# Performance work log

Measured on AMD Instinct MI355X. Metric: run time of the kernel, lower is better.

The kernel has to match this reference:

```python
import jax, jax.numpy as jnp
import numpy as np

def setup_inputs() -> dict:
    key = jax.random.key(0)
    x = jax.random.normal(key, (4, 1, 192, 224, 192), dtype=jnp.float32)
    return {"x": x}

def reference(x) -> jnp.ndarray:
    # Zero-pad each spatial dim by 1 (matches F.conv3d padding=1),
    # then take central differences: out[i] = (x[i+1] - x[i-1]) / 2.
    xp = jnp.pad(x, ((0, 0), (0, 0), (1, 1), (1, 1), (1, 1)))
    half = jnp.asarray(0.5, dtype=x.dtype)
    dz = (xp[:, :, 2:, 1:-1, 1:-1] - xp[:, :, :-2, 1:-1, 1:-1]) * half  # D axis (dZ kernel)
    dy = (xp[:, :, 1:-1, 2:, 1:-1] - xp[:, :, 1:-1, :-2, 1:-1]) * half  # H axis (dY kernel)
    dx = (xp[:, :, 1:-1, 1:-1, 2:] - xp[:, :, 1:-1, 1:-1, :-2]) * half  # W axis (dX kernel)
    return jnp.abs(dx) + jnp.abs(dy) + jnp.abs(dz)
```

## Files before the change

### kernel.cpp

```cpp
#include <hip/hip_runtime.h>


constexpr int W = 192, H = 224, D = 192, B = 4;
constexpr int W4     = W / 4;
constexpr int PLANE4 = W4 * H;
constexpr int BY     = 4;
constexpr int CH     = 2;
constexpr int ZC     = D / CH;
constexpr int YT     = H / BY;
constexpr int GRID   = B * ZC * YT;
constexpr int PERX   = GRID / 8;

typedef float f32x4 __attribute__((ext_vector_type(4)));

__global__ __launch_bounds__(192) void grad3d_kernel(
    const float* __restrict__ in, float* __restrict__ out) {
    int bid = blockIdx.x;
    int sid = (bid & 7) * PERX + (bid >> 3);
    const int yt = sid % YT; sid /= YT;
    const int zc = sid % ZC; sid /= ZC;
    const int b  = sid;

    const int xv = threadIdx.x;
    const int r  = yt * BY + threadIdx.y;
    const int z0 = zc * CH;

    const f32x4* __restrict__ in4 = (const f32x4*)in;
    f32x4* __restrict__ out4 = (f32x4*)out;
    const f32x4 zf = {0.f, 0.f, 0.f, 0.f};

    const bool has_l  = (xv > 0);
    const bool has_r  = (xv < W4 - 1);
    const bool has_ym = (r > 0);
    const bool has_yp = (r < H - 1);

    const int i0 = (b * D + z0) * PLANE4 + r * W4 + xv;
    const int i1 = i0 + PLANE4;

    f32x4 czm = (z0 > 0)     ? in4[i0 - PLANE4] : zf;
    f32x4 c0  =                in4[i0];
    f32x4 c1  =                in4[i1];
    f32x4 czp = (z0 + 2 < D) ? in4[i1 + PLANE4] : zf;
    f32x4 ym0 = has_ym ? in4[i0 - W4] : zf;
    f32x4 yp0 = has_yp ? in4[i0 + W4] : zf;
    f32x4 ym1 = has_ym ? in4[i1 - W4] : zf;
    f32x4 yp1 = has_yp ? in4[i1 + W4] : zf;
    float l0  = has_l ? in[i0 * 4 - 1] : 0.f;
    float r0e = has_r ? in[i0 * 4 + 4] : 0.f;
    float l1  = has_l ? in[i1 * 4 - 1] : 0.f;
    float r1e = has_r ? in[i1 * 4 + 4] : 0.f;

    f32x4 o0, o1;
    o0.x = fabsf((c0.y - l0  ) * .5f) + fabsf((yp0.x - ym0.x) * .5f) + fabsf((c1.x - czm.x) * .5f);
    o0.y = fabsf((c0.z - c0.x) * .5f) + fabsf((yp0.y - ym0.y) * .5f) + fabsf((c1.y - czm.y) * .5f);
    o0.z = fabsf((c0.w - c0.y) * .5f) + fabsf((yp0.z - ym0.z) * .5f) + fabsf((c1.z - czm.z) * .5f);
    o0.w = fabsf((r0e  - c0.z) * .5f) + fabsf((yp0.w - ym0.w) * .5f) + fabsf((c1.w - czm.w) * .5f);
    o1.x = fabsf((c1.y - l1  ) * .5f) + fabsf((yp1.x - ym1.x) * .5f) + fabsf((czp.x - c0.x) * .5f);
    o1.y = fabsf((c1.z - c1.x) * .5f) + fabsf((yp1.y - ym1.y) * .5f) + fabsf((czp.y - c0.y) * .5f);
    o1.z = fabsf((c1.w - c1.y) * .5f) + fabsf((yp1.z - ym1.z) * .5f) + fabsf((czp.z - c0.z) * .5f);
    o1.w = fabsf((r1e  - c1.z) * .5f) + fabsf((yp1.w - ym1.w) * .5f) + fabsf((czp.w - c0.w) * .5f);

    __builtin_nontemporal_store(o0, out4 + i0);
    __builtin_nontemporal_store(o1, out4 + i1);
}

extern "C" void kernel_launch(void* const* d_in, const int* in_sizes, int n_in,
                              void* d_out, int out_size, void* d_ws, size_t ws_size,
                              hipStream_t stream) {
    const float* x = (const float*)d_in[0];
    float* out     = (float*)d_out;
    dim3 block(W4, BY);
    grad3d_kernel<<<GRID, block, 0, stream>>>(x, out);
}
```

Before: 242.1 us.

## Stage halo tile in LDS via direct global-to-LDS loads for 3D stencil

Each block now stages an 8x10 plane halo tile (6 z-slices plus halos, 8 rows plus halos, full width) into shared memory using global_load_lds async loads, then computes 6 z-planes per thread from LDS. This cuts the redundant global reads of neighbour rows and planes that the register-only version issued. In exchange it adds a block-wide barrier and about 60 KB of LDS per block, which limits occupancy, and the load and compute phases no longer overlap within a block.

```diff
diff --git a/kernel.cpp b/kernel.cpp
--- a/kernel.cpp
+++ b/kernel.cpp
@@ -2,66 +2,100 @@
 
 
 constexpr int W = 192, H = 224, D = 192, B = 4;
-constexpr int W4     = W / 4;
-constexpr int PLANE4 = W4 * H;
-constexpr int BY     = 4;
-constexpr int CH     = 2;
-constexpr int ZC     = D / CH;
-constexpr int YT     = H / BY;
-constexpr int GRID   = B * ZC * YT;
-constexpr int PERX   = GRID / 8;
+constexpr int W4   = W / 4;
+constexpr int ZT   = 6, YT = 8;
+constexpr int ZP   = ZT + 2;
+constexpr int YP   = YT + 2;
+constexpr int ROWB = W * 4;
+constexpr int PLB  = YP * ROWB;
+constexpr int LDSB = ZP * PLB;
+constexpr int NZ   = D / ZT;
+constexpr int NY   = H / YT;
+constexpr int GRID = B * NZ * NY;
+constexpr int PERX = GRID / 8;
 
 typedef float f32x4 __attribute__((ext_vector_type(4)));
+typedef __attribute__((address_space(3))) unsigned int       lds_u32;
+typedef __attribute__((address_space(1))) const unsigned int gbl_u32;
 
-__global__ __launch_bounds__(192) void grad3d_kernel(
+__global__ __launch_bounds__(384) void grad3d_kernel(
     const float* __restrict__ in, float* __restrict__ out) {
+    __shared__ float s[LDSB / 4];
+
     int bid = blockIdx.x;
     int sid = (bid & 7) * PERX + (bid >> 3);
-    const int yt = sid % YT; sid /= YT;
-    const int zc = sid % ZC; sid /= ZC;
+    const int yt = sid % NY; sid /= NY;
+    const int zc = sid % NZ; sid /= NZ;
     const int b  = sid;
 
-    const int xv = threadIdx.x;
-    const int r  = yt * BY + threadIdx.y;
-    const int z0 = zc * CH;
+    const int xv   = threadIdx.x;
+    const int y    = threadIdx.y;
+    const int flat = y * W4 + xv;
+    const int wv   = flat >> 6;
+    const int lane = flat & 63;
 
-    const f32x4* __restrict__ in4 = (const f32x4*)in;
-    f32x4* __restrict__ out4 = (f32x4*)out;
+    const int y0 = yt * YT;
+    const int z0 = zc * ZT;
+    const bool ybot = (y0 == 0);
+    const bool ytop = (y0 + YT == H);
+
+    f32x4* s4 = (f32x4*)s;
     const f32x4 zf = {0.f, 0.f, 0.f, 0.f};
 
-    const bool has_l  = (xv > 0);
-    const bool has_r  = (xv < W4 - 1);
-    const bool has_ym = (r > 0);
-    const bool has_yp = (r < H - 1);
+    if (z0 == 0)
+        for (int i = flat; i < PLB / 16; i += 384) s4[i] = zf;
+    if (z0 + ZT == D)
+        for (int i = flat; i < PLB / 16; i += 384) s4[(LDSB - PLB) / 16 + i] = zf;
+    if (ybot)
+        s4[y * (PLB / 16) + xv] = zf;
+    if (ytop)
+        s4[y * (PLB / 16) + (YP - 1) * W4 + xv] = zf;
 
-    const int i0 = (b * D + z0) * PLANE4 + r * W4 + xv;
-    const int i1 = i0 + PLANE4;
+    const char* inb = (const char*)in;
+    for (int c = wv; c < 64; c += 6) {
+        const int zz = c >> 3;
+        const int j  = c & 7;
+        const int gz = z0 - 1 + zz;
+        if (gz < 0 || gz >= D) continue;
+        const int p = (j << 10) + (lane << 4);
+        bool ok = (p < PLB);
+        if (ybot && p < ROWB)       ok = false;
+        if (ytop && p >= PLB - ROWB) ok = false;
+        if (ok) {
+            const char* g = inb + (size_t)((b * D + gz) * H + (y0 - 1)) * ROWB + p;
+            unsigned int* l = (unsigned int*)((char*)s + zz * PLB + (j << 10));
+            __builtin_amdgcn_global_load_lds((gbl_u32*)g, (lds_u32*)l, 16, 0, 0);
+        }
+    }
 
-    f32x4 czm = (z0 > 0)     ? in4[i0 - PLANE4] : zf;
-    f32x4 c0  =                in4[i0];
-    f32x4 c1  =                in4[i1];
-    f32x4 czp = (z0 + 2 < D) ? in4[i1 + PLANE4] : zf;
-    f32x4 ym0 = has_ym ? in4[i0 - W4] : zf;
-    f32x4 yp0 = has_yp ? in4[i0 + W4] : zf;
-    f32x4 ym1 = has_ym ? in4[i1 - W4] : zf;
-    f32x4 yp1 = has_yp ? in4[i1 + W4] : zf;
-    float l0  = has_l ? in[i0 * 4 - 1] : 0.f;
-    float r0e = has_r ? in[i0 * 4 + 4] : 0.f;
-    float l1  = has_l ? in[i1 * 4 - 1] : 0.f;
-    float r1e = has_r ? in[i1 * 4 + 4] : 0.f;
+    __syncthreads();
 
-    f32x4 o0, o1;
-    o0.x = fabsf((c0.y - l0  ) * .5f) + fabsf((yp0.x - ym0.x) * .5f) + fabsf((c1.x - czm.x) * .5f);
-    o0.y = fabsf((c0.z - c0.x) * .5f) + fabsf((yp0.y - ym0.y) * .5f) + fabsf((c1.y - czm.y) * .5f);
-    o0.z = fabsf((c0.w - c0.y) * .5f) + fabsf((yp0.z - ym0.z) * .5f) + fabsf((c1.z - czm.z) * .5f);
-    o0.w = fabsf((r0e  - c0.z) * .5f) + fabsf((yp0.w - ym0.w) * .5f) + fabsf((c1.w - czm.w) * .5f);
-    o1.x = fabsf((c1.y - l1  ) * .5f) + fabsf((yp1.x - ym1.x) * .5f) + fabsf((czp.x - c0.x) * .5f);
-    o1.y = fabsf((c1.z - c1.x) * .5f) + fabsf((yp1.y - ym1.y) * .5f) + fabsf((czp.y - c0.y) * .5f);
-    o1.z = fabsf((c1.w - c1.y) * .5f) + fabsf((yp1.z - ym1.z) * .5f) + fabsf((czp.z - c0.z) * .5f);
-    o1.w = fabsf((r1e  - c1.z) * .5f) + fabsf((yp1.w - ym1.w) * .5f) + fabsf((czp.w - c0.w) * .5f);
+    f32x4* out4 = (f32x4*)out;
+    constexpr int rowf = W;
+    constexpr int plf  = YP * W;
+    int ci = (YP + (y + 1)) * rowf + 4 * xv;
+    size_t oi = ((size_t)(b * D + z0) * H + (y0 + y)) * W4 + xv;
 
-    __builtin_nontemporal_store(o0, out4 + i0);
-    __builtin_nontemporal_store(o1, out4 + i1);
+#pragma unroll
+    for (int z = 0; z < ZT; ++z) {
+        f32x4 cc = *(const f32x4*)&s[ci];
+        f32x4 ym = *(const f32x4*)&s[ci - rowf];
+        f32x4 yp = *(const f32x4*)&s[ci + rowf];
+        f32x4 zm = *(const f32x4*)&s[ci - plf];
+        f32x4 zp = *(const f32x4*)&s[ci + plf];
+        float l  = (xv > 0)      ? s[ci - 1] : 0.f;
+        float r  = (xv < W4 - 1) ? s[ci + 4] : 0.f;
+
+        f32x4 o;
+        o.x = fabsf((cc.y - l   ) * .5f) + fabsf((yp.x - ym.x) * .5f) + fabsf((zp.x - zm.x) * .5f);
+        o.y = fabsf((cc.z - cc.x) * .5f) + fabsf((yp.y - ym.y) * .5f) + fabsf((zp.y - zm.y) * .5f);
+        o.z = fabsf((cc.w - cc.y) * .5f) + fabsf((yp.z - ym.z) * .5f) + fabsf((zp.z - zm.z) * .5f);
+        o.w = fabsf((r    - cc.z) * .5f) + fabsf((yp.w - ym.w) * .5f) + fabsf((zp.w - zm.w) * .5f);
+        __builtin_nontemporal_store(o, out4 + oi);
+
+        ci += plf;
+        oi += (size_t)H * W4;
+    }
 }
 
 extern "C" void kernel_launch(void* const* d_in, const int* in_sizes, int n_in,
@@ -69,6 +103,6 @@
                               hipStream_t stream) {
     const float* x = (const float*)d_in[0];
     float* out     = (float*)d_out;
-    dim3 block(W4, BY);
+    dim3 block(W4, YT);
     grad3d_kernel<<<GRID, block, 0, stream>>>(x, out);
 }
```

Result: faster. 231.8 us (-4.2%).

## Stream z-planes through an LDS ring buffer with async global_load_lds prefetch

Applied to the files above, without the earlier changes.

Replaces the one-shot per-thread stencil with blocks that march 16 z-planes over a 14-row y tile. Each plane is loaded once into a 4-slot LDS ring with direct global-to-LDS loads, prefetched two planes ahead, and reused for neighbor reads, with lane shuffles supplying the x neighbors. The goal is to cut redundant global reads (z and y halos) and overlap loads with compute. The cost is manual vmcnt waits, two barriers per plane, and fewer, longer-running blocks.

```diff
diff --git a/kernel.cpp b/kernel.cpp
--- a/kernel.cpp
+++ b/kernel.cpp
@@ -3,65 +3,125 @@
 
 constexpr int W = 192, H = 224, D = 192, B = 4;
 constexpr int W4     = W / 4;
-constexpr int PLANE4 = W4 * H;
-constexpr int BY     = 4;
-constexpr int CH     = 2;
-constexpr int ZC     = D / CH;
-constexpr int YT     = H / BY;
-constexpr int GRID   = B * ZC * YT;
+constexpr int YT     = 14;
+constexpr int YR     = YT + 2;
+constexpr int ROWB   = W * 4;
+constexpr int SLOTB  = YR * ROWB;
+constexpr int SLOTFL = SLOTB / 4;
+constexpr int SLOTF4 = SLOTB / 16;
+constexpr int ZL     = 16;
+constexpr int NYT    = H / YT;
+constexpr int NZC    = D / ZL;
+constexpr int GRID   = B * NYT * NZC;
 constexpr int PERX   = GRID / 8;
+constexpr int NTHR   = 256;
+constexpr int NF4    = YT * W4;
 
 typedef float f32x4 __attribute__((ext_vector_type(4)));
+typedef __attribute__((address_space(3))) unsigned int       lds_u32;
+typedef __attribute__((address_space(1))) const unsigned int gbl_u32;
 
-__global__ __launch_bounds__(192) void grad3d_kernel(
+#define WAITV(N) asm volatile("s_waitcnt vmcnt(" #N ")" ::: "memory")
+#define WAITLG   asm volatile("s_waitcnt lgkmcnt(0)" ::: "memory")
+#define BARR     asm volatile("s_barrier" ::: "memory")
+
+__global__ __launch_bounds__(NTHR) void grad3d_kernel(
     const float* __restrict__ in, float* __restrict__ out) {
+    __shared__ float s[4 * SLOTFL];
+
     int bid = blockIdx.x;
     int sid = (bid & 7) * PERX + (bid >> 3);
-    const int yt = sid % YT; sid /= YT;
-    const int zc = sid % ZC; sid /= ZC;
-    const int b  = sid;
+    const int ytile = sid % NYT; sid /= NYT;
+    const int zc    = sid % NZC; sid /= NZC;
+    const int b     = sid;
 
-    const int xv = threadIdx.x;
-    const int r  = yt * BY + threadIdx.y;
-    const int z0 = zc * CH;
+    const int tid  = threadIdx.x;
+    const int wv   = tid >> 6;
+    const int lane = tid & 63;
+    const int z0   = zc * ZL;
+    const int y0   = ytile * YT;
+    const bool ybot = (ytile == 0), ytop = (ytile == NYT - 1);
 
-    const f32x4* __restrict__ in4 = (const f32x4*)in;
-    f32x4* __restrict__ out4 = (f32x4*)out;
+    f32x4* s4 = (f32x4*)s;
+    f32x4* out4 = (f32x4*)out;
     const f32x4 zf = {0.f, 0.f, 0.f, 0.f};
+    const char* inb = (const char*)in;
 
-    const bool has_l  = (xv > 0);
-    const bool has_r  = (xv < W4 - 1);
-    const bool has_ym = (r > 0);
-    const bool has_yp = (r < H - 1);
+    if (ybot) for (int i = tid; i < 4 * W4; i += NTHR)
+        s4[(i / W4) * SLOTF4 + (i % W4)] = zf;
+    if (ytop) for (int i = tid; i < 4 * W4; i += NTHR)
+        s4[(i / W4) * SLOTF4 + (YR - 1) * W4 + (i % W4)] = zf;
 
-    const int i0 = (b * D + z0) * PLANE4 + r * W4 + xv;
-    const int i1 = i0 + PLANE4;
+    auto STAGE = [&](int q) {
+        const int sl = (q + 4) & 3;
+        if (q < 0 || q >= D) {
+            #pragma unroll
+            for (int k = 0; k < 3; ++k)
+                s4[sl * SLOTF4 + k * NTHR + tid] = zf;
+            return;
+        }
+        const char* gbase = inb + (size_t)((b * D + q) * H + (y0 - 1)) * ROWB;
+        char* lbase = (char*)s + sl * SLOTB;
+        #pragma unroll
+        for (int k = 0; k < 3; ++k) {
+            const int c   = 3 * wv + k;
+            const int off = (c << 10) + (lane << 4);
+            bool ok = true;
+            if (ybot && off < ROWB)         ok = false;
+            if (ytop && off >= SLOTB - ROWB) ok = false;
+            if (ok)
+                __builtin_amdgcn_global_load_lds(
+                    (gbl_u32*)(gbase + off),
+                    (lds_u32*)(lbase + (c << 10)), 16, 0, 0);
+        }
+    };
 
-    f32x4 czm = (z0 > 0)     ? in4[i0 - PLANE4] : zf;
-    f32x4 c0  =                in4[i0];
-    f32x4 c1  =                in4[i1];
-    f32x4 czp = (z0 + 2 < D) ? in4[i1 + PLANE4] : zf;
-    f32x4 ym0 = has_ym ? in4[i0 - W4] : zf;
-    f32x4 yp0 = has_yp ? in4[i0 + W4] : zf;
-    f32x4 ym1 = has_ym ? in4[i1 - W4] : zf;
-    f32x4 yp1 = has_yp ? in4[i1 + W4] : zf;
-    float l0  = has_l ? in[i0 * 4 - 1] : 0.f;
-    float r0e = has_r ? in[i0 * 4 + 4] : 0.f;
-    float l1  = has_l ? in[i1 * 4 - 1] : 0.f;
-    float r1e = has_r ? in[i1 * 4 + 4] : 0.f;
+    STAGE(z0 - 1);
+    STAGE(z0);
+    STAGE(z0 + 1);
 
-    f32x4 o0, o1;
-    o0.x = fabsf((c0.y - l0  ) * .5f) + fabsf((yp0.x - ym0.x) * .5f) + fabsf((c1.x - czm.x) * .5f);
-    o0.y = fabsf((c0.z - c0.x) * .5f) + fabsf((yp0.y - ym0.y) * .5f) + fabsf((c1.y - czm.y) * .5f);
-    o0.z = fabsf((c0.w - c0.y) * .5f) + fabsf((yp0.z - ym0.z) * .5f) + fabsf((c1.z - czm.z) * .5f);
-    o0.w = fabsf((r0e  - c0.z) * .5f) + fabsf((yp0.w - ym0.w) * .5f) + fabsf((c1.w - czm.w) * .5f);
-    o1.x = fabsf((c1.y - l1  ) * .5f) + fabsf((yp1.x - ym1.x) * .5f) + fabsf((czp.x - c0.x) * .5f);
-    o1.y = fabsf((c1.z - c1.x) * .5f) + fabsf((yp1.y - ym1.y) * .5f) + fabsf((czp.y - c0.y) * .5f);
-    o1.z = fabsf((c1.w - c1.y) * .5f) + fabsf((yp1.z - ym1.z) * .5f) + fabsf((czp.z - c0.z) * .5f);
-    o1.w = fabsf((r1e  - c1.z) * .5f) + fabsf((yp1.w - ym1.w) * .5f) + fabsf((czp.w - c0.w) * .5f);
+    for (int t = 0; t < ZL; ++t) {
+        const int z = z0 + t;
+        const int q = z + 2;
+        const bool inr = (q < D);
+        STAGE(q);
+        if (t == 0)      WAITV(3);
+        else if (inr)    WAITV(5);
+        else             WAITV(2);
+        WAITLG;
+        BARR;
 
-    __builtin_nontemporal_store(o0, out4 + i0);
-    __builtin_nontemporal_store(o1, out4 + i1);
+        const int szm = (z + 3) & 3, sz = z & 3, szp = (z + 1) & 3;
+        #pragma unroll
+        for (int it = 0; it < 3; ++it) {
+            const int f = it * NTHR + tid;
+            if (f < NF4) {
+                const int row = f / W4, xv = f % W4;
+                const int bf  = (row + 1) * W + 4 * xv;
+                f32x4 cc = *(const f32x4*)&s[sz  * SLOTFL + bf];
+                f32x4 ym = *(const f32x4*)&s[sz  * SLOTFL + bf - W];
+                f32x4 yp = *(const f32x4*)&s[sz  * SLOTFL + bf + W];
+                f32x4 zm = *(const f32x4*)&s[szm * SLOTFL + bf];
+                f32x4 zp = *(const f32x4*)&s[szp * SLOTFL + bf];
+
+                float l = __shfl_up(cc.w, 1);
+                float r = __shfl_down(cc.x, 1);
+                if (lane == 0  && xv > 0)      l = s[sz * SLOTFL + bf - 1];
+                if (lane == 63 && xv < W4 - 1) r = s[sz * SLOTFL + bf + 4];
+                if (xv == 0)      l = 0.f;
+                if (xv == W4 - 1) r = 0.f;
+
+                f32x4 o;
+                o.x = fabsf((cc.y - l   ) * .5f) + fabsf((yp.x - ym.x) * .5f) + fabsf((zp.x - zm.x) * .5f);
+                o.y = fabsf((cc.z - cc.x) * .5f) + fabsf((yp.y - ym.y) * .5f) + fabsf((zp.y - zm.y) * .5f);
+                o.z = fabsf((cc.w - cc.y) * .5f) + fabsf((yp.z - ym.z) * .5f) + fabsf((zp.z - zm.z) * .5f);
+                o.w = fabsf((r    - cc.z) * .5f) + fabsf((yp.w - ym.w) * .5f) + fabsf((zp.w - zm.w) * .5f);
+                __builtin_nontemporal_store(
+                    o, out4 + ((size_t)(b * D + z) * H + (y0 + row)) * W4 + xv);
+            }
+        }
+        BARR;
+    }
 }
 
 extern "C" void kernel_launch(void* const* d_in, const int* in_sizes, int n_in,
@@ -69,6 +129,5 @@
                               hipStream_t stream) {
     const float* x = (const float*)d_in[0];
     float* out     = (float*)d_out;
-    dim3 block(W4, BY);
-    grad3d_kernel<<<GRID, block, 0, stream>>>(x, out);
+    grad3d_kernel<<<GRID, NTHR, 0, stream>>>(x, out);
 }
```

After: 237.4 us. Within noise of the previous version (-1.9%).
